# Kernel optimization log

Hardware: AMD Instinct MI355X
Metric: run time of the kernel (lower is better)

Reference implementation:

```python
import jax, jax.numpy as jnp
import numpy as np

HIDDEN = 2048
NUM_HEADS = 8
NUM_KV_HEADS = 2
HEAD_DIM = 256
ROPE_BASE = 1e6
EPS = 1e-6
B, S = 2, 2048


def rms_norm(x, w, eps=EPS):
    # normalize over last dim (head_dim), per-head
    var = jnp.mean(jnp.square(x), axis=-1, keepdims=True)
    return x * jax.lax.rsqrt(var + eps) * w


def rope(x, positions, base=ROPE_BASE):
    # neox-style rotate-half RoPE over full head_dim. x: [B,S,H,D], positions: [B,S]
    d = x.shape[-1]
    inv_freq = 1.0 / (base ** (jnp.arange(0, d, 2, dtype=jnp.float32) / d))
    freqs = positions.astype(jnp.float32)[..., None] * inv_freq  # [B,S,D/2]
    cos = jnp.cos(freqs)[:, :, None, :]
    sin = jnp.sin(freqs)[:, :, None, :]
    x1, x2 = x[..., : d // 2], x[..., d // 2 :]
    return jnp.concatenate([x1 * cos - x2 * sin, x2 * cos + x1 * sin], axis=-1)


def setup_inputs() -> dict:
    key = jax.random.key(0)
    k1, k2, k3 = jax.random.split(key, 3)
    hidden_states = jax.random.normal(k1, (B, S, HIDDEN), dtype=jnp.float32)
    positions = jnp.broadcast_to(jnp.arange(S, dtype=jnp.int32), (B, S))
    qkv_out = (NUM_HEADS + 2 * NUM_KV_HEADS) * HEAD_DIM
    w_qkv = jax.random.normal(k2, (HIDDEN, qkv_out), dtype=jnp.float32) * (HIDDEN ** -0.5)
    w_o = jax.random.normal(k3, (NUM_HEADS * HEAD_DIM, HIDDEN), dtype=jnp.float32) * ((NUM_HEADS * HEAD_DIM) ** -0.5)
    q_norm_w = jnp.ones((HEAD_DIM,), dtype=jnp.float32)
    k_norm_w = jnp.ones((HEAD_DIM,), dtype=jnp.float32)
    return {"hidden_states": hidden_states, "positions": positions, "w_qkv": w_qkv,
            "w_o": w_o, "q_norm_w": q_norm_w, "k_norm_w": k_norm_w}


def reference(hidden_states, positions, w_qkv, w_o, q_norm_w, k_norm_w):
    b, s, _ = hidden_states.shape
    q_size = NUM_HEADS * HEAD_DIM
    kv_size = NUM_KV_HEADS * HEAD_DIM
    qkv = hidden_states @ w_qkv  # [B,S,q+2kv]
    q, k, v = jnp.split(qkv, [q_size, q_size + kv_size], axis=-1)
    q = q.reshape(b, s, NUM_HEADS, HEAD_DIM)
    k = k.reshape(b, s, NUM_KV_HEADS, HEAD_DIM)
    v = v.reshape(b, s, NUM_KV_HEADS, HEAD_DIM)
    # per-head RMSNorm; v_norm has no learned scale (weight fixed to ones)
    q = rms_norm(q, q_norm_w)
    k = rms_norm(k, k_norm_w)
    v = rms_norm(v, jnp.ones((HEAD_DIM,), dtype=v.dtype))
    # RoPE
    q = rope(q, positions)
    k = rope(k, positions)
    # GQA: repeat kv heads
    g = NUM_HEADS // NUM_KV_HEADS
    k = jnp.repeat(k, g, axis=2)
    v = jnp.repeat(v, g, axis=2)
    # causal attention with scaling = 1.0 (as in module)
    scores = jnp.einsum("bqhd,bkhd->bhqk", q, k)
    mask = jnp.tril(jnp.ones((s, s), dtype=bool))
    scores = jnp.where(mask, scores, jnp.finfo(scores.dtype).min)
    probs = jax.nn.softmax(scores, axis=-1)
    attn = jnp.einsum("bhqk,bkhd->bqhd", probs, v).reshape(b, s, NUM_HEADS * HEAD_DIM)
    return attn @ w_o
```

## Files before the change

kernel.cpp:

```cpp
#include <hip/hip_runtime.h>


#define HID  2048
#define NH   8
#define NKV  2
#define HD   256
#define SB   2048
#define BB   2
#define MTOK (BB * SB)
#define NQKV ((NH + 2 * NKV) * HD)

typedef _Float16  f16x8 __attribute__((ext_vector_type(8)));
typedef float     f32x4 __attribute__((ext_vector_type(4)));

__device__ __forceinline__ unsigned short f2h(float f) {
  _Float16 h = (_Float16)f;
  return __builtin_bit_cast(unsigned short, h);
}

__device__ __forceinline__ void async_copy16(const unsigned short* g, unsigned short* l) {
  __builtin_amdgcn_global_load_lds(
      (const __attribute__((address_space(1))) unsigned int*)g,
      (__attribute__((address_space(3))) unsigned int*)l, 16, 0, 0);
}

__device__ __forceinline__ int swz4(int r) { return (r + (r >> 2)) & 3; }

template <int MODE, int BN>
__global__ __launch_bounds__(512, 2) void gemm_p2(const unsigned short* __restrict__ A,
                                                  const unsigned short* __restrict__ Bt,
                                                  void* __restrict__ Cg,
                                                  int M, int N, int K,
                                                  const int* __restrict__ pos,
                                                  const float* __restrict__ qw,
                                                  const float* __restrict__ kw,
                                                  unsigned short* __restrict__ Qh,
                                                  unsigned short* __restrict__ Kh,
                                                  unsigned short* __restrict__ Vt) {
  constexpr int WN  = BN / 4;
  constexpr int NF  = BN / 64;
  constexpr int LPTB = BN / 128;
  __shared__ __align__(16) unsigned short SMG[4 * 256 * 32 + 4 * BN * 32];
  unsigned short* Ash = SMG;
  unsigned short* Bsh = SMG + 4 * 256 * 32;

  const int t = threadIdx.x;
  const int lane = t & 63, w = t >> 6;
  const int quad = lane >> 4, m15 = lane & 15;
  const int wm = w >> 2, wn = w & 3;

  const int nwg = gridDim.x * gridDim.y;
  int bid = blockIdx.y * gridDim.x + blockIdx.x;
  if ((nwg & 7) == 0) bid = (bid & 7) * (nwg >> 3) + (bid >> 3);
  const int bx = bid % gridDim.x, by = bid / gridDim.x;
  const int m0 = by * 256, n0 = bx * BN;

  const unsigned short* aSrc[2];
  int aDst[2];
#pragma unroll
  for (int j = 0; j < 2; ++j) {
    const int c = t + j * 512;
    const int row = c >> 2, slot = c & 3;
    aSrc[j] = A + (size_t)(m0 + row) * K + ((slot ^ swz4(row)) * 8);
    aDst[j] = c * 8;
  }
  const unsigned short* bSrc[LPTB];
  int bDst[LPTB];
#pragma unroll
  for (int j = 0; j < LPTB; ++j) {
    const int c = t + j * 512;
    const int row = c >> 2, slot = c & 3;
    bSrc[j] = Bt + (size_t)(n0 + row) * K + ((slot ^ swz4(row)) * 8);
    bDst[j] = c * 8;
  }

  int offA[8], offB[NF];
#pragma unroll
  for (int i = 0; i < 8; ++i) {
    const int ra = wm * 128 + i * 16 + m15;
    offA[i] = ra * 32 + ((quad ^ swz4(ra)) * 8);
  }
#pragma unroll
  for (int j = 0; j < NF; ++j) {
    const int rb = wn * WN + j * 16 + m15;
    offB[j] = rb * 32 + ((quad ^ swz4(rb)) * 8);
  }

  const f32x4 vz = {0.f, 0.f, 0.f, 0.f};
  f32x4 acc[8][NF];
#pragma unroll
  for (int i = 0; i < 8; ++i)
#pragma unroll
    for (int j = 0; j < NF; ++j) acc[i][j] = vz;

  const int NK = K >> 5;

  for (int pt = 0; pt < 3; ++pt) {
    const int kb = pt * 32;
    unsigned short* ab = &Ash[pt * 8192];
    unsigned short* bb = &Bsh[pt * (BN * 32)];
#pragma unroll
    for (int j = 0; j < 2; ++j) async_copy16(aSrc[j] + kb, ab + aDst[j]);
#pragma unroll
    for (int j = 0; j < LPTB; ++j) async_copy16(bSrc[j] + kb, bb + bDst[j]);
  }
  if constexpr (BN == 256) asm volatile("s_waitcnt vmcnt(8)" ::: "memory");
  else                     asm volatile("s_waitcnt vmcnt(6)" ::: "memory");
  __builtin_amdgcn_s_barrier();

  for (int kt = 0; kt < NK; ++kt) {
    const int buf = kt & 3;
    const unsigned short* Ab = &Ash[buf * 8192];
    const unsigned short* Bb = &Bsh[buf * (BN * 32)];
    const int s3 = kt + 3;
    const int kb3 = s3 * 32;
    unsigned short* a3 = &Ash[(s3 & 3) * 8192];
    unsigned short* b3 = &Bsh[(s3 & 3) * (BN * 32)];
    const bool stage3 = (s3 < NK);

    f16x8 af[4], bf[NF];
#pragma unroll
    for (int i = 0; i < 4; ++i) af[i] = *(const f16x8*)&Ab[offA[i]];
#pragma unroll
    for (int j = 0; j < NF; ++j) bf[j] = *(const f16x8*)&Bb[offB[j]];
    if (stage3) {
#pragma unroll
      for (int j = 0; j < 2; ++j) async_copy16(aSrc[j] + kb3, a3 + aDst[j]);
    }
    __builtin_amdgcn_s_barrier();
    asm volatile("s_waitcnt lgkmcnt(0)" ::: "memory");
    __builtin_amdgcn_sched_barrier(0);
    __builtin_amdgcn_s_setprio(1);
#pragma unroll
    for (int i = 0; i < 4; ++i)
#pragma unroll
      for (int j = 0; j < NF; ++j)
        acc[i][j] = __builtin_amdgcn_mfma_f32_16x16x32_f16(af[i], bf[j], acc[i][j], 0, 0, 0);
    __builtin_amdgcn_s_setprio(0);
    __builtin_amdgcn_s_barrier();

    f16x8 ag[4];
#pragma unroll
    for (int i = 0; i < 4; ++i) ag[i] = *(const f16x8*)&Ab[offA[4 + i]];
    if (stage3) {
#pragma unroll
      for (int j = 0; j < LPTB; ++j) async_copy16(bSrc[j] + kb3, b3 + bDst[j]);
    }
    __builtin_amdgcn_s_barrier();
    asm volatile("s_waitcnt lgkmcnt(0)" ::: "memory");
    __builtin_amdgcn_sched_barrier(0);
    __builtin_amdgcn_s_setprio(1);
#pragma unroll
    for (int i = 0; i < 4; ++i)
#pragma unroll
      for (int j = 0; j < NF; ++j)
        acc[4 + i][j] = __builtin_amdgcn_mfma_f32_16x16x32_f16(ag[i], bf[j], acc[4 + i][j], 0, 0, 0);
    __builtin_amdgcn_s_setprio(0);
    if (stage3) {
      if constexpr (BN == 256) asm volatile("s_waitcnt vmcnt(8)" ::: "memory");
      else                     asm volatile("s_waitcnt vmcnt(6)" ::: "memory");
    } else {
      asm volatile("s_waitcnt vmcnt(0)" ::: "memory");
    }
    __builtin_amdgcn_s_barrier();
  }

  if constexpr (MODE == 2) {
#pragma unroll
    for (int i = 0; i < 8; ++i)
#pragma unroll
      for (int j = 0; j < NF; ++j)
#pragma unroll
        for (int r = 0; r < 4; ++r) {
          const int gm = m0 + wm * 128 + i * 16 + quad * 4 + r;
          const int gn = n0 + wn * WN + j * 16 + m15;
          ((float*)Cg)[(size_t)gm * N + gn] = acc[i][j][r];
        }
  } else {
    const int st = (bx < 8) ? 0 : (bx < 10 ? 1 : 2);
    constexpr int ES = 260;
    const int dbase = lane * 4;
    const bool lo = (lane < 32);

    for (int half = 0; half < 2; ++half) {
      if (wm == half) {
#pragma unroll
        for (int i = 0; i < 8; ++i)
#pragma unroll
          for (int j = 0; j < NF; ++j)
#pragma unroll
            for (int r = 0; r < 4; ++r)
              SMG[(i * 16 + quad * 4 + r) * ES + wn * 64 + j * 16 + m15] = f2h(acc[i][j][r]);
      }
      __syncthreads();

#pragma unroll
      for (int ti = 0; ti < 16; ++ti) {
        const int tl = w * 16 + ti;
        const int gtok = m0 + half * 128 + tl;
        const int b = gtok >> 11, s = gtok & 2047;
        union { uint2 u; _Float16 h[4]; } rd;
        rd.u = *(const uint2*)&SMG[tl * ES + dbase];
        float y[4];
#pragma unroll
        for (int e = 0; e < 4; ++e) y[e] = (float)rd.h[e];
        float ssq = y[0] * y[0] + y[1] * y[1] + y[2] * y[2] + y[3] * y[3];
#pragma unroll
        for (int off = 1; off < 64; off <<= 1) ssq += __shfl_xor(ssq, off);
        const float rn = rsqrtf(ssq * (1.f / 256.f) + 1e-6f);

        if (st == 0) {
#pragma unroll
          for (int e = 0; e < 4; ++e) y[e] *= rn * qw[dbase + e];
        } else if (st == 1) {
#pragma unroll
          for (int e = 0; e < 4; ++e) y[e] *= rn * kw[dbase + e];
        } else {
#pragma unroll
          for (int e = 0; e < 4; ++e) y[e] *= rn;
        }

        union { uint2 u; _Float16 h[4]; } wr;
        if (st < 2) {
          const float p = (float)pos[gtok];
          const int i0 = dbase & 127;
#pragma unroll
          for (int e = 0; e < 4; ++e) {
            const float partner = __shfl_xor(y[e], 32);
            const float invf = __expf(-(float)(i0 + e) * 0.10793368f);
            const float fr = p * invf;
            const float cv = __cosf(fr), sv = __sinf(fr);
            wr.h[e] = (_Float16)(lo ? (y[e] * cv - partner * sv)
                                    : (y[e] * cv + partner * sv));
          }
          unsigned short* dst = (st == 0)
              ? Qh + ((size_t)(b * NH + bx) * SB + s) * HD + dbase
              : Kh + ((size_t)(b * NKV + (bx - 8)) * SB + s) * HD + dbase;
          *(uint2*)dst = wr.u;
        } else {
#pragma unroll
          for (int e = 0; e < 4; ++e) wr.h[e] = (_Float16)y[e];
          *(uint2*)&SMG[tl * ES + dbase] = wr.u;
        }
      }

      if (st == 2) {
        __syncthreads();
        const int kv = bx - 10;
#pragma unroll
        for (int rep = 0; rep < 32; ++rep) {
          const int d = w + 8 * rep;
          const int tp = lane * 2;
          const unsigned short vlo = SMG[tp * ES + d];
          const unsigned short vhi = SMG[(tp + 1) * ES + d];
          const int gs = m0 + half * 128 + tp;
          const int b = gs >> 11, s = gs & 2047;
          const int s5 = s & 31;
          const int sp = (s & ~31) | (((s5 >> 2) & 3) << 3) | (((s5 >> 4) & 1) << 2) | (s5 & 3);
          *(unsigned int*)&Vt[((size_t)(b * NKV + kv) * HD + d) * SB + sp] =
              (unsigned)vlo | ((unsigned)vhi << 16);
        }
      }
      __syncthreads();
    }
  }
}

__global__ __launch_bounds__(256) void prep(const float* __restrict__ hidden,
                                            unsigned short* __restrict__ hb,
                                            const float* __restrict__ w_qkv,
                                            unsigned short* __restrict__ wqkvT,
                                            const float* __restrict__ w_o,
                                            unsigned short* __restrict__ woT) {
  __shared__ float tile[64 * 68];
  const int bid = blockIdx.x;
  const int t = threadIdx.x;

  if (bid < 8192) {
    const int i = bid * 256 + t;
    const float4 v = ((const float4*)hidden)[i];
    ushort4 o = {f2h(v.x), f2h(v.y), f2h(v.z), f2h(v.w)};
    ((ushort4*)hb)[i] = o;
    return;
  }

  const float* in;
  unsigned short* out;
  int R, C, r0, c0;
  if (bid < 9728) {
    const int bb = bid - 8192;
    in = w_qkv; out = wqkvT; R = HID; C = NQKV;
    r0 = (bb / 48) * 64; c0 = (bb % 48) * 64;
  } else {
    const int bb = bid - 9728;
    in = w_o; out = woT; R = HID; C = HID;
    r0 = (bb / 32) * 64; c0 = (bb % 32) * 64;
  }
#pragma unroll
  for (int p = 0; p < 4; ++p) {
    const int idx = t + p * 256;
    const int rr = idx >> 4, cc = (idx & 15) * 4;
    *(float4*)&tile[rr * 68 + cc] = *(const float4*)&in[(size_t)(r0 + rr) * C + c0 + cc];
  }
  __syncthreads();
#pragma unroll
  for (int p = 0; p < 2; ++p) {
    const int idx = t + p * 256;
    const int dr = idx >> 3, sc = (idx & 7) * 8;
    union { uint4 v; unsigned short s[8]; } o;
#pragma unroll
    for (int e = 0; e < 8; ++e) o.s[e] = f2h(tile[(sc + e) * 68 + dr]);
    *(uint4*)&out[(size_t)(c0 + dr) * R + r0 + sc] = o.v;
  }
}

__global__ __launch_bounds__(512, 2) void flash_attn(const unsigned short* __restrict__ Qh,
                                                     const unsigned short* __restrict__ Kh,
                                                     const unsigned short* __restrict__ Vt,
                                                     unsigned short* __restrict__ attn) {
  __shared__ __align__(16) unsigned char SMEM[132096];
  unsigned short* Ksh = (unsigned short*)SMEM;
  unsigned short* Vsh = (unsigned short*)(SMEM + 65536);
  float*         MLx  = (float*)(SMEM + 131072);
  float*         mergeO = (float*)SMEM;

  const int pairi = blockIdx.x;
  const int h = blockIdx.y, b = blockIdx.z;
  const int kv = h >> 2;
  const int t = threadIdx.x, w = t >> 6, lane = t & 63;
  const int wq = w & 3, team = w >> 2;
  const int quad = lane >> 4, m15 = lane & 15;

  const unsigned short* Kb = Kh + (size_t)(b * NKV + kv) * SB * HD;
  const unsigned short* Vb = Vt + (size_t)(b * NKV + kv) * HD * SB;

  const int krow = t >> 5, kchunk = t & 31;
  const int vrow = t >> 3, vchunk = t & 7;

  const f32x4 vz = {0.f, 0.f, 0.f, 0.f};

  for (int jb = 0; jb < 2; ++jb) {
    const int qt = jb ? (31 - pairi) : pairi;
    const int q0 = qt * 64, qw0 = q0 + wq * 16;
    const int qlane = qw0 + m15;

    f16x8 aq[8];
    const unsigned short* qb = Qh + ((size_t)(b * NH + h) * SB + qw0 + m15) * HD + quad * 8;
#pragma unroll
    for (int ks = 0; ks < 8; ++ks) aq[ks] = *(const f16x8*)(qb + ks * 32);

    f32x4 o[16];
#pragma unroll
    for (int i = 0; i < 16; ++i) o[i] = vz;
    float mrow = -1e30f, lrow = 0.f;

    const int nkt = (q0 + 64) >> 6;

#pragma unroll
    for (int shot = 0; shot < 4; ++shot) {
      const int r = krow + 16 * shot;
      async_copy16(Kb + (size_t)r * HD + ((kchunk ^ (r & 7)) * 8),
                   &Ksh[4096 * shot + t * 8]);
    }
#pragma unroll
    for (int shot = 0; shot < 4; ++shot) {
      const int d = vrow + 64 * shot;
      async_copy16(Vb + (size_t)d * SB + ((vchunk ^ (d & 7)) * 8),
                   &Vsh[4096 * shot + t * 8]);
    }
    __syncthreads();

    for (int kt = 0; kt < nkt; ++kt) {
      const int k0 = kt * 64;
      const int par = kt & 1;

      if (kt + 1 < nkt) {
        const int kn = k0 + 64;
        const int pn = par ^ 1;
#pragma unroll
        for (int shot = 0; shot < 4; ++shot) {
          const int r = krow + 16 * shot;
          async_copy16(Kb + (size_t)(kn + r) * HD + ((kchunk ^ (r & 7)) * 8),
                       &Ksh[pn * 16384 + 4096 * shot + t * 8]);
        }
#pragma unroll
        for (int shot = 0; shot < 4; ++shot) {
          const int d = vrow + 64 * shot;
          async_copy16(Vb + (size_t)d * SB + kn + ((vchunk ^ (d & 7)) * 8),
                       &Vsh[pn * 16384 + 4096 * shot + t * 8]);
        }
      }

      const unsigned short* KB = &Ksh[par * 16384];
      const unsigned short* VB = &Vsh[par * 16384];

      f32x4 sv[2];
      sv[0] = vz; sv[1] = vz;
      __builtin_amdgcn_s_setprio(1);
#pragma unroll
      for (int g = 0; g < 2; ++g) {
        const int key = team * 32 + g * 16 + m15;
        const unsigned short* kr = &KB[key * 256];
        const int sw = (key & 7);
#pragma unroll
        for (int ks = 0; ks < 8; ++ks) {
          const f16x8 ak = *(const f16x8*)&kr[((4 * ks + quad) ^ sw) * 8];
          sv[g] = __builtin_amdgcn_mfma_f32_16x16x32_f16(ak, aq[ks], sv[g], 0, 0, 0);
        }
      }
      __builtin_amdgcn_s_setprio(0);

      const bool last = (kt == nkt - 1);
      float p2[2][4];
#pragma unroll
      for (int g = 0; g < 2; ++g)
#pragma unroll
        for (int r = 0; r < 4; ++r) {
          float s = sv[g][r];
          if (last && (k0 + team * 32 + g * 16 + quad * 4 + r) > qlane) s = -3.0e38f;
          p2[g][r] = s;
        }
      float tm = fmaxf(fmaxf(fmaxf(p2[0][0], p2[0][1]), fmaxf(p2[0][2], p2[0][3])),
                       fmaxf(fmaxf(p2[1][0], p2[1][1]), fmaxf(p2[1][2], p2[1][3])));
      tm = fmaxf(tm, __shfl_xor(tm, 16));
      tm = fmaxf(tm, __shfl_xor(tm, 32));
      if (!__all(tm <= mrow)) {
        const float mnew = fmaxf(mrow, tm);
        const float alpha = __expf(mrow - mnew);
        lrow *= alpha;
#pragma unroll
        for (int dbi = 0; dbi < 16; ++dbi) o[dbi] *= alpha;
        mrow = mnew;
      }
      float rs = 0.f;
#pragma unroll
      for (int g = 0; g < 2; ++g)
#pragma unroll
        for (int r = 0; r < 4; ++r) { p2[g][r] = __expf(p2[g][r] - mrow); rs += p2[g][r]; }
      rs += __shfl_xor(rs, 16);
      rs += __shfl_xor(rs, 32);
      lrow += rs;

      f16x8 bp;
#pragma unroll
      for (int g = 0; g < 2; ++g)
#pragma unroll
        for (int r = 0; r < 4; ++r) bp[g * 4 + r] = (_Float16)p2[g][r];

      __builtin_amdgcn_s_setprio(1);
#pragma unroll
      for (int dbi = 0; dbi < 16; ++dbi) {
        const int d = dbi * 16 + m15;
        const f16x8 av = *(const f16x8*)&VB[d * 64 + (((team * 4 + quad) ^ (d & 7)) * 8)];
        o[dbi] = __builtin_amdgcn_mfma_f32_16x16x32_f16(av, bp, o[dbi], 0, 0, 0);
      }
      __builtin_amdgcn_s_setprio(0);

      __syncthreads();
    }

    if (quad == 0) {
      MLx[w * 32 + m15 * 2]     = mrow;
      MLx[w * 32 + m15 * 2 + 1] = lrow;
    }
    {
      float* mo = mergeO + w * 2176;
#pragma unroll
      for (int ii = 0; ii < 8; ++ii) {
        const int dbi = team ? ii : (8 + ii);
#pragma unroll
        for (int r = 0; r < 4; ++r)
          mo[(ii * 16 + quad * 4 + r) * 17 + m15] = o[dbi][r];
      }
    }
    __syncthreads();
    {
      const int pw = w ^ 4;
      const float* pmo = mergeO + pw * 2176;
      const float pm = MLx[pw * 32 + m15 * 2];
      const float pl = MLx[pw * 32 + m15 * 2 + 1];
      const float mm = fmaxf(mrow, pm);
      const float a0 = __expf(mrow - mm);
      const float a1 = __expf(pm - mm);
      const float invl = 1.0f / (a0 * lrow + a1 * pl);
      const int q = qlane;
#pragma unroll
      for (int ii = 0; ii < 8; ++ii) {
        const int dbi = team ? (8 + ii) : ii;
        union { uint2 u; _Float16 hh[4]; } st;
#pragma unroll
        for (int r = 0; r < 4; ++r) {
          const float po = pmo[(ii * 16 + quad * 4 + r) * 17 + m15];
          st.hh[r] = (_Float16)((a0 * o[dbi][r] + a1 * po) * invl);
        }
        const int dcol = team * 128 + ii * 16 + quad * 4;
        *(uint2*)&attn[(size_t)(b * SB + q) * (NH * HD) + h * HD + dcol] = st.u;
      }
    }
    __syncthreads();
  }
}

static constexpr size_t OFF_QH   = 0;
static constexpr size_t OFF_KH   = 16777216;
static constexpr size_t OFF_VT   = 20971520;
static constexpr size_t OFF_W1T  = 25165824;
static constexpr size_t OFF_WOT  = 37748736;
static constexpr size_t OFF_HB   = 46137344;
static constexpr size_t OFF_ATTN = OFF_HB;

extern "C" void kernel_launch(void* const* d_in, const int* in_sizes, int n_in,
                              void* d_out, int out_size, void* d_ws, size_t ws_size,
                              hipStream_t stream) {
  const float* hidden    = (const float*)d_in[0];
  const int*   positions = (const int*)d_in[1];
  const float* w_qkv     = (const float*)d_in[2];
  const float* w_o       = (const float*)d_in[3];
  const float* qw        = (const float*)d_in[4];
  const float* kw        = (const float*)d_in[5];
  float* out = (float*)d_out;
  char* ws = (char*)d_ws;

  unsigned short* hb    = (unsigned short*)(ws + OFF_HB);
  unsigned short* wqkvT = (unsigned short*)(ws + OFF_W1T);
  unsigned short* woT   = (unsigned short*)(ws + OFF_WOT);
  unsigned short* attnb = (unsigned short*)(ws + OFF_ATTN);
  unsigned short* Qhb   = (unsigned short*)(ws + OFF_QH);
  unsigned short* Khb   = (unsigned short*)(ws + OFF_KH);
  unsigned short* Vtb   = (unsigned short*)(ws + OFF_VT);

  prep<<<dim3(10752), 256, 0, stream>>>(hidden, hb, w_qkv, wqkvT, w_o, woT);

  gemm_p2<3, 256><<<dim3(NQKV / 256, MTOK / 256), 512, 0, stream>>>(
      hb, wqkvT, nullptr, MTOK, NQKV, HID, positions, qw, kw, Qhb, Khb, Vtb);

  flash_attn<<<dim3(16, NH, BB), 512, 0, stream>>>(Qhb, Khb, Vtb, attnb);

  gemm_p2<2, 128><<<dim3(HID / 128, MTOK / 256), 512, 0, stream>>>(
      attnb, woT, out, MTOK, HID, HID, nullptr, nullptr, nullptr, nullptr, nullptr, nullptr);
}
```

Measured before the change: 318.2 us.

## Fuse prep, QKV GEMM, attention and output GEMM into one cooperative kernel

Replaces four kernel launches with a single cooperative persistent kernel of 256 blocks that runs each stage in turn, separated by grid-wide syncs. The prep stage is reshaped so each block loops over a fixed share of the conversion and transpose work. This is meant to remove launch gaps and per-kernel ramp-up and tail costs. In exchange, every block uses the large shared memory allocation of the attention stage in every phase. The QKV GEMM leaves 64 blocks idle, and the grid syncs add barrier latency plus load imbalance at each stage boundary.

```diff
diff --git a/kernel.cpp b/kernel.cpp
--- a/kernel.cpp
+++ b/kernel.cpp
@@ -1,4 +1,7 @@
 #include <hip/hip_runtime.h>
+#include <hip/hip_cooperative_groups.h>
+
+namespace cg = cooperative_groups;
 
 
 #define HID  2048
@@ -26,21 +29,81 @@
 
 __device__ __forceinline__ int swz4(int r) { return (r + (r >> 2)) & 3; }
 
+static constexpr size_t OFF_QH   = 0;
+static constexpr size_t OFF_KH   = 16777216;
+static constexpr size_t OFF_VT   = 20971520;
+static constexpr size_t OFF_W1T  = 25165824;
+static constexpr size_t OFF_WOT  = 37748736;
+static constexpr size_t OFF_HB   = 46137344;
+static constexpr size_t OFF_ATTN = OFF_HB;
+
+__device__ void prep_body(unsigned char* SMraw, int blk,
+                          const float* __restrict__ hidden,
+                          unsigned short* __restrict__ hb,
+                          const float* __restrict__ w_qkv,
+                          unsigned short* __restrict__ wqkvT,
+                          const float* __restrict__ w_o,
+                          unsigned short* __restrict__ woT) {
+  float* tile = (float*)SMraw;
+  const int t = threadIdx.x;
+
+  {
+    const int base = blk * 512 + t;
+#pragma unroll
+    for (int it = 0; it < 16; ++it) {
+      const int i = base + it * 131072;
+      const float4 v = ((const float4*)hidden)[i];
+      ushort4 o = {f2h(v.x), f2h(v.y), f2h(v.z), f2h(v.w)};
+      ((ushort4*)hb)[i] = o;
+    }
+  }
+
+  for (int it = 0; it < 10; ++it) {
+    const int tid = blk * 10 + it;
+    const float* in;
+    unsigned short* out;
+    int R, C, r0, c0;
+    if (tid < 1536) {
+      in = w_qkv; out = wqkvT; R = HID; C = NQKV;
+      r0 = (tid / 48) * 64; c0 = (tid % 48) * 64;
+    } else {
+      const int bb = tid - 1536;
+      in = w_o; out = woT; R = HID; C = HID;
+      r0 = (bb / 32) * 64; c0 = (bb % 32) * 64;
+    }
+    __syncthreads();
+#pragma unroll
+    for (int p = 0; p < 2; ++p) {
+      const int idx = t + p * 512;
+      const int rr = idx >> 4, cc = (idx & 15) * 4;
+      *(float4*)&tile[rr * 68 + cc] = *(const float4*)&in[(size_t)(r0 + rr) * C + c0 + cc];
+    }
+    __syncthreads();
+    {
+      const int dr = t >> 3, sc = (t & 7) * 8;
+      union { uint4 v; unsigned short s[8]; } o;
+#pragma unroll
+      for (int e = 0; e < 8; ++e) o.s[e] = f2h(tile[(sc + e) * 68 + dr]);
+      *(uint4*)&out[(size_t)(c0 + dr) * R + r0 + sc] = o.v;
+    }
+  }
+}
+
 template <int MODE, int BN>
-__global__ __launch_bounds__(512, 2) void gemm_p2(const unsigned short* __restrict__ A,
-                                                  const unsigned short* __restrict__ Bt,
-                                                  void* __restrict__ Cg,
-                                                  int M, int N, int K,
-                                                  const int* __restrict__ pos,
-                                                  const float* __restrict__ qw,
-                                                  const float* __restrict__ kw,
-                                                  unsigned short* __restrict__ Qh,
-                                                  unsigned short* __restrict__ Kh,
-                                                  unsigned short* __restrict__ Vt) {
+__device__ void gemm_body(unsigned short* SMG, int bid0, int gx, int nwg,
+                          const unsigned short* __restrict__ A,
+                          const unsigned short* __restrict__ Bt,
+                          void* __restrict__ Cg,
+                          int M, int N, int K,
+                          const int* __restrict__ pos,
+                          const float* __restrict__ qw,
+                          const float* __restrict__ kw,
+                          unsigned short* __restrict__ Qh,
+                          unsigned short* __restrict__ Kh,
+                          unsigned short* __restrict__ Vt) {
   constexpr int WN  = BN / 4;
   constexpr int NF  = BN / 64;
   constexpr int LPTB = BN / 128;
-  __shared__ __align__(16) unsigned short SMG[4 * 256 * 32 + 4 * BN * 32];
   unsigned short* Ash = SMG;
   unsigned short* Bsh = SMG + 4 * 256 * 32;
 
@@ -49,10 +112,9 @@
   const int quad = lane >> 4, m15 = lane & 15;
   const int wm = w >> 2, wn = w & 3;
 
-  const int nwg = gridDim.x * gridDim.y;
-  int bid = blockIdx.y * gridDim.x + blockIdx.x;
+  int bid = bid0;
   if ((nwg & 7) == 0) bid = (bid & 7) * (nwg >> 3) + (bid >> 3);
-  const int bx = bid % gridDim.x, by = bid / gridDim.x;
+  const int bx = bid % gx, by = bid / gx;
   const int m0 = by * 256, n0 = bx * BN;
 
   const unsigned short* aSrc[2];
@@ -266,66 +328,16 @@
   }
 }
 
-__global__ __launch_bounds__(256) void prep(const float* __restrict__ hidden,
-                                            unsigned short* __restrict__ hb,
-                                            const float* __restrict__ w_qkv,
-                                            unsigned short* __restrict__ wqkvT,
-                                            const float* __restrict__ w_o,
-                                            unsigned short* __restrict__ woT) {
-  __shared__ float tile[64 * 68];
-  const int bid = blockIdx.x;
-  const int t = threadIdx.x;
-
-  if (bid < 8192) {
-    const int i = bid * 256 + t;
-    const float4 v = ((const float4*)hidden)[i];
-    ushort4 o = {f2h(v.x), f2h(v.y), f2h(v.z), f2h(v.w)};
-    ((ushort4*)hb)[i] = o;
-    return;
-  }
-
-  const float* in;
-  unsigned short* out;
-  int R, C, r0, c0;
-  if (bid < 9728) {
-    const int bb = bid - 8192;
-    in = w_qkv; out = wqkvT; R = HID; C = NQKV;
-    r0 = (bb / 48) * 64; c0 = (bb % 48) * 64;
-  } else {
-    const int bb = bid - 9728;
-    in = w_o; out = woT; R = HID; C = HID;
-    r0 = (bb / 32) * 64; c0 = (bb % 32) * 64;
-  }
-#pragma unroll
-  for (int p = 0; p < 4; ++p) {
-    const int idx = t + p * 256;
-    const int rr = idx >> 4, cc = (idx & 15) * 4;
-    *(float4*)&tile[rr * 68 + cc] = *(const float4*)&in[(size_t)(r0 + rr) * C + c0 + cc];
-  }
-  __syncthreads();
-#pragma unroll
-  for (int p = 0; p < 2; ++p) {
-    const int idx = t + p * 256;
-    const int dr = idx >> 3, sc = (idx & 7) * 8;
-    union { uint4 v; unsigned short s[8]; } o;
-#pragma unroll
-    for (int e = 0; e < 8; ++e) o.s[e] = f2h(tile[(sc + e) * 68 + dr]);
-    *(uint4*)&out[(size_t)(c0 + dr) * R + r0 + sc] = o.v;
-  }
-}
-
-__global__ __launch_bounds__(512, 2) void flash_attn(const unsigned short* __restrict__ Qh,
-                                                     const unsigned short* __restrict__ Kh,
-                                                     const unsigned short* __restrict__ Vt,
-                                                     unsigned short* __restrict__ attn) {
-  __shared__ __align__(16) unsigned char SMEM[132096];
+__device__ void flash_body(unsigned char* SMEM, int pairi, int h, int b,
+                           const unsigned short* __restrict__ Qh,
+                           const unsigned short* __restrict__ Kh,
+                           const unsigned short* __restrict__ Vt,
+                           unsigned short* __restrict__ attn) {
   unsigned short* Ksh = (unsigned short*)SMEM;
   unsigned short* Vsh = (unsigned short*)(SMEM + 65536);
   float*         MLx  = (float*)(SMEM + 131072);
   float*         mergeO = (float*)SMEM;
 
-  const int pairi = blockIdx.x;
-  const int h = blockIdx.y, b = blockIdx.z;
   const int kv = h >> 2;
   const int t = threadIdx.x, w = t >> 6, lane = t & 63;
   const int wq = w & 3, team = w >> 2;
@@ -501,13 +513,44 @@
   }
 }
 
-static constexpr size_t OFF_QH   = 0;
-static constexpr size_t OFF_KH   = 16777216;
-static constexpr size_t OFF_VT   = 20971520;
-static constexpr size_t OFF_W1T  = 25165824;
-static constexpr size_t OFF_WOT  = 37748736;
-static constexpr size_t OFF_HB   = 46137344;
-static constexpr size_t OFF_ATTN = OFF_HB;
+__global__ __launch_bounds__(512, 2) void mega(const float* __restrict__ hidden,
+                                               const int* __restrict__ pos,
+                                               const float* __restrict__ w_qkv,
+                                               const float* __restrict__ w_o,
+                                               const float* __restrict__ qw,
+                                               const float* __restrict__ kw,
+                                               float* __restrict__ out,
+                                               unsigned char* __restrict__ ws) {
+  __shared__ __align__(16) unsigned char SM[132096];
+
+  unsigned short* hb    = (unsigned short*)(ws + OFF_HB);
+  unsigned short* wqkvT = (unsigned short*)(ws + OFF_W1T);
+  unsigned short* woT   = (unsigned short*)(ws + OFF_WOT);
+  unsigned short* attnb = (unsigned short*)(ws + OFF_ATTN);
+  unsigned short* Qhb   = (unsigned short*)(ws + OFF_QH);
+  unsigned short* Khb   = (unsigned short*)(ws + OFF_KH);
+  unsigned short* Vtb   = (unsigned short*)(ws + OFF_VT);
+
+  const int blk = blockIdx.x;
+  cg::grid_group grid = cg::this_grid();
+
+  prep_body(SM, blk, hidden, hb, w_qkv, wqkvT, w_o, woT);
+  __threadfence();
+  grid.sync();
+
+  if (blk < 192)
+    gemm_body<3, 256>((unsigned short*)SM, blk, 12, 192, hb, wqkvT, nullptr,
+                      MTOK, NQKV, HID, pos, qw, kw, Qhb, Khb, Vtb);
+  __threadfence();
+  grid.sync();
+
+  flash_body(SM, blk & 15, (blk >> 4) & 7, blk >> 7, Qhb, Khb, Vtb, attnb);
+  __threadfence();
+  grid.sync();
+
+  gemm_body<2, 128>((unsigned short*)SM, blk, 16, 256, attnb, woT, out,
+                    MTOK, HID, HID, nullptr, nullptr, nullptr, nullptr, nullptr, nullptr);
+}
 
 extern "C" void kernel_launch(void* const* d_in, const int* in_sizes, int n_in,
                               void* d_out, int out_size, void* d_ws, size_t ws_size,
@@ -519,23 +562,10 @@
   const float* qw        = (const float*)d_in[4];
   const float* kw        = (const float*)d_in[5];
   float* out = (float*)d_out;
-  char* ws = (char*)d_ws;
-
-  unsigned short* hb    = (unsigned short*)(ws + OFF_HB);
-  unsigned short* wqkvT = (unsigned short*)(ws + OFF_W1T);
-  unsigned short* woT   = (unsigned short*)(ws + OFF_WOT);
-  unsigned short* attnb = (unsigned short*)(ws + OFF_ATTN);
-  unsigned short* Qhb   = (unsigned short*)(ws + OFF_QH);
-  unsigned short* Khb   = (unsigned short*)(ws + OFF_KH);
-  unsigned short* Vtb   = (unsigned short*)(ws + OFF_VT);
-
-  prep<<<dim3(10752), 256, 0, stream>>>(hidden, hb, w_qkv, wqkvT, w_o, woT);
-
-  gemm_p2<3, 256><<<dim3(NQKV / 256, MTOK / 256), 512, 0, stream>>>(
-      hb, wqkvT, nullptr, MTOK, NQKV, HID, positions, qw, kw, Qhb, Khb, Vtb);
-
-  flash_attn<<<dim3(16, NH, BB), 512, 0, stream>>>(Qhb, Khb, Vtb, attnb);
-
-  gemm_p2<2, 128><<<dim3(HID / 128, MTOK / 256), 512, 0, stream>>>(
-      attnb, woT, out, MTOK, HID, HID, nullptr, nullptr, nullptr, nullptr, nullptr, nullptr);
-}
+  unsigned char* wsu = (unsigned char*)d_ws;
+
+  void* args[] = {(void*)&hidden, (void*)&positions, (void*)&w_qkv, (void*)&w_o,
+                  (void*)&qw, (void*)&kw, (void*)&out, (void*)&wsu};
+  hipLaunchCooperativeKernel(reinterpret_cast<void*>(mega), dim3(256), dim3(512),
+                             args, 0, stream);
+}
```

After: 580.1 us. 1.82x slower.
